# Optimization experiments

Measured on AMD Instinct MI355X. Metric: run time of the kernel, lower is better.

Reference implementation:

```python
import jax, jax.numpy as jnp
import numpy as np

N = 8192
IN_F = 512
OUT_F = 128
NUM_CLASSES = 10
ALPHA = 0.2  # LeakyReLU negative slope
NEG_INF = -9e15


def setup_inputs() -> dict:
    key = jax.random.key(0)
    k_h, k_d, k_W, k_a, k_cw, k_cb = jax.random.split(key, 6)
    h = jax.random.normal(k_h, (N, IN_F), dtype=jnp.float32)
    dist = jax.random.randint(k_d, (N, N), 0, 2, dtype=jnp.int32)
    # xavier_uniform with gain=1.414
    gain = 1.414
    lim_W = gain * np.sqrt(6.0 / (IN_F + OUT_F))
    W = jax.random.uniform(k_W, (IN_F, OUT_F), minval=-lim_W, maxval=lim_W, dtype=jnp.float32)
    lim_a = gain * np.sqrt(6.0 / (2 * OUT_F + 1))
    a = jax.random.uniform(k_a, (2 * OUT_F, 1), minval=-lim_a, maxval=lim_a, dtype=jnp.float32)
    # nn.Linear(out_features, num_classes): weight [C, out], bias [C]
    lim_c = np.sqrt(1.0 / OUT_F)
    Wc = jax.random.uniform(k_cw, (NUM_CLASSES, OUT_F), minval=-lim_c, maxval=lim_c, dtype=jnp.float32)
    bc = jax.random.uniform(k_cb, (NUM_CLASSES,), minval=-lim_c, maxval=lim_c, dtype=jnp.float32)
    return {"h": h, "dist": dist, "W": W, "a": a, "Wc": Wc, "bc": bc}


def reference(h, dist, W, a, Wc, bc):
    Wh = h @ W                              # [N, out]
    Wh1 = Wh @ a[:OUT_F]                    # [N, 1]
    Wh2 = Wh @ a[OUT_F:]                    # [N, 1]
    e = jax.nn.leaky_relu(Wh1 + Wh2.T, negative_slope=ALPHA)  # [N, N]
    att = jnp.where(dist > 0, e, NEG_INF)
    att = jax.nn.softmax(att, axis=1)       # [N, N]
    h_update = jax.nn.elu(att @ Wh)         # [N, out] (dropout inactive at inference)
    y_pred = h_update @ Wc.T + bc           # [N, num_classes]
    return y_pred
```

## Files before the change

### kernel.cpp

```cpp
#include <hip/hip_runtime.h>
#include <stdint.h>

#define N 8192
#define IN_F 512
#define OUT_F 128
#define NCLS 10
#define ALPHA 0.2f

#define WCOLS 1024
#define NSP (N / WCOLS)
#define BK 128
#define NIT (WCOLS / BK)
#define MSTR 33

typedef float f32x4 __attribute__((ext_vector_type(4)));
typedef int   i32x4 __attribute__((ext_vector_type(4)));
typedef short s16x8 __attribute__((ext_vector_type(8)));

__device__ __forceinline__ short f2bf(float x) {
    unsigned u = __builtin_bit_cast(unsigned, x);
    u = (u + 0x7FFFu + ((u >> 16) & 1u)) >> 16;
    return (short)u;
}
__device__ __forceinline__ float bf2f(short s) {
    unsigned u = ((unsigned)(unsigned short)s) << 16;
    return __builtin_bit_cast(float, u);
}

__global__ void split_w_kernel(const float* __restrict__ W,
                               short* __restrict__ WThi, short* __restrict__ WTlo) {
    int idx = blockIdx.x * 256 + threadIdx.x;
    int k = idx >> 7, col = idx & 127;
    float x = W[idx];
    short hi = f2bf(x);
    short lo = f2bf(x - bf2f(hi));
    size_t a = (size_t)(k >> 5) * (128 * 32) + (size_t)col * 32 + (k & 31);
    WThi[a] = hi;
    WTlo[a] = lo;
}

#define WH_ROWS 16
#define WH_STR 520

__global__ __launch_bounds__(256, 2)
void wh_kernel(const float* __restrict__ h, const short* __restrict__ WThi,
               const short* __restrict__ WTlo, const float* __restrict__ a,
               short* __restrict__ WhT, float* __restrict__ Wh1,
               float* __restrict__ Wh2) {
    __shared__ __align__(16) short Ahi[WH_ROWS][WH_STR];
    __shared__ __align__(16) short Alo[WH_ROWS][WH_STR];
    __shared__ __align__(16) float whs[WH_ROWS][OUT_F + 4];

    const int t = threadIdx.x;
    const int r0 = blockIdx.x * WH_ROWS;

    {
        int row = t >> 4, c4 = t & 15;
        const float* hrow = h + (size_t)(r0 + row) * IN_F;
        #pragma unroll
        for (int jj = 0; jj < 4; ++jj) {
            int k0 = c4 * 8 + jj * 128;
            f32x4 x0 = *(const f32x4*)(hrow + k0);
            f32x4 x1 = *(const f32x4*)(hrow + k0 + 4);
            s16x8 hi, lo;
            #pragma unroll
            for (int e = 0; e < 4; ++e) {
                short h0 = f2bf(x0[e]); hi[e] = h0; lo[e] = f2bf(x0[e] - bf2f(h0));
                short h1 = f2bf(x1[e]); hi[4 + e] = h1; lo[4 + e] = f2bf(x1[e] - bf2f(h1));
            }
            *(s16x8*)&Ahi[row][k0] = hi;
            *(s16x8*)&Alo[row][k0] = lo;
        }
    }
    __syncthreads();

    const int lane = t & 63, w = t >> 6;
    const int q = lane >> 4, ln16 = lane & 15;
    f32x4 acc[2] = {};
    #pragma unroll
    for (int kc = 0; kc < IN_F / 32; ++kc) {
        s16x8 ahi = *(const s16x8*)&Ahi[ln16][kc * 32 + q * 8];
        s16x8 alo = *(const s16x8*)&Alo[ln16][kc * 32 + q * 8];
        #pragma unroll
        for (int nt = 0; nt < 2; ++nt) {
            int col = w * 32 + nt * 16 + ln16;
            size_t boff = (size_t)kc * 4096 + (size_t)col * 32 + q * 8;
            s16x8 bhi = *(const s16x8*)(WThi + boff);
            s16x8 blo = *(const s16x8*)(WTlo + boff);
            acc[nt] = __builtin_amdgcn_mfma_f32_16x16x32_bf16(ahi, bhi, acc[nt], 0, 0, 0);
            acc[nt] = __builtin_amdgcn_mfma_f32_16x16x32_bf16(ahi, blo, acc[nt], 0, 0, 0);
            acc[nt] = __builtin_amdgcn_mfma_f32_16x16x32_bf16(alo, bhi, acc[nt], 0, 0, 0);
        }
    }
    #pragma unroll
    for (int nt = 0; nt < 2; ++nt)
        #pragma unroll
        for (int reg = 0; reg < 4; ++reg)
            whs[q * 4 + reg][w * 32 + nt * 16 + ln16] = acc[nt][reg];
    __syncthreads();

    if (t < 128) {
        int r = t >> 3, s = t & 7;
        float s1 = 0.f, s2 = 0.f;
        #pragma unroll
        for (int cc = 0; cc < 16; ++cc) {
            int c = s * 16 + cc;
            float v = whs[r][c];
            s1 = fmaf(v, a[c], s1);
            s2 = fmaf(v, a[OUT_F + c], s2);
        }
        s1 += __shfl_xor(s1, 1); s1 += __shfl_xor(s1, 2); s1 += __shfl_xor(s1, 4);
        s2 += __shfl_xor(s2, 1); s2 += __shfl_xor(s2, 2); s2 += __shfl_xor(s2, 4);
        if (s == 0) { Wh1[r0 + r] = s1; Wh2[r0 + r] = s2; }
    }

    {
        int c = t >> 1, h8 = t & 1;
        s16x8 pack;
        #pragma unroll
        for (int rr = 0; rr < 8; ++rr) pack[rr] = f2bf(whs[h8 * 8 + rr][c]);
        size_t addr = (size_t)(r0 >> 5) * 4096 + (size_t)c * 32 + (r0 & 16) + h8 * 8;
        *(s16x8*)(WhT + addr) = pack;
    }
}

__global__ __launch_bounds__(256, 4)
void attn_kernel(const int* __restrict__ dist, const short* __restrict__ WhT,
                 const float* __restrict__ Wh1v, const float* __restrict__ Wh2v,
                 float* __restrict__ acc_part, float* __restrict__ l_part) {
    __shared__ unsigned maskL[64 * MSTR];
    __shared__ __align__(16) float wh2L[WCOLS];

    const int t = threadIdx.x;
    const int it = blockIdx.x & 127;
    const int sp = blockIdx.x >> 7;
    const int i0 = it * 64;
    const int j0 = sp * WCOLS;
    const int lane = t & 63, w = t >> 6;
    const int q = lane >> 4, m = lane & 15;

    {
        const int l = lane;
        #pragma unroll 4
        for (int rr = 0; rr < 16; ++rr) {
            const int r = w * 16 + rr;
            const int* rp = dist + (size_t)(i0 + r) * N + j0 + l * 4;
            #pragma unroll
            for (int p = 0; p < 4; ++p) {
                i32x4 v = *(const i32x4*)(rp + p * 256);
                unsigned nib = (unsigned)(v[0] > 0) | ((unsigned)(v[1] > 0) << 1)
                             | ((unsigned)(v[2] > 0) << 2) | ((unsigned)(v[3] > 0) << 3);
                unsigned b = nib | (__shfl_xor(nib, 1) << 4);
                b = b | (__shfl_xor(b, 2) << 8);
                b = b | (__shfl_xor(b, 4) << 16);
                if ((l & 7) == 0) maskL[r * MSTR + p * 8 + (l >> 3)] = b;
            }
        }
        if (t < WCOLS / 4)
            *(f32x4*)&wh2L[t * 4] = *(const f32x4*)(Wh2v + j0 + t * 4);
    }
    __syncthreads();

    const int row = i0 + w * 16 + m;
    const float wh1 = Wh1v[row];
    float l_acc = 0.f;
    f32x4 acc[8] = {};
    const unsigned* mrow = &maskL[(w * 16 + m) * MSTR];

    for (int kt = 0; kt < NIT; ++kt) {
        const int jb = kt * BK;
        s16x8 afr[4];
        #pragma unroll
        for (int kc = 0; kc < 4; ++kc) {
            unsigned mw = mrow[(jb >> 5) + kc];
            unsigned byq = (mw >> (q * 8)) & 255u;
            f32x4 w20 = *(const f32x4*)&wh2L[jb + kc * 32 + q * 8];
            f32x4 w21 = *(const f32x4*)&wh2L[jb + kc * 32 + q * 8 + 4];
            #pragma unroll
            for (int e = 0; e < 4; ++e) {
                float sv = wh1 + w20[e];
                float lr = fmaxf(sv, ALPHA * sv);
                float pv = ((byq >> e) & 1u) ? __expf(lr) : 0.f;
                l_acc += pv;
                afr[kc][e] = (short)((__builtin_bit_cast(unsigned, pv) + 0x8000u) >> 16);
                float sv1 = wh1 + w21[e];
                float lr1 = fmaxf(sv1, ALPHA * sv1);
                float pv1 = ((byq >> (4 + e)) & 1u) ? __expf(lr1) : 0.f;
                l_acc += pv1;
                afr[kc][4 + e] = (short)((__builtin_bit_cast(unsigned, pv1) + 0x8000u) >> 16);
            }
        }
        const short* bb = WhT + (size_t)((j0 + jb) >> 5) * 4096 + q * 8;
        #pragma unroll
        for (int kc = 0; kc < 4; ++kc) {
            const short* bkc = bb + (size_t)kc * 4096;
            #pragma unroll
            for (int nt = 0; nt < 8; ++nt) {
                s16x8 bfr = *(const s16x8*)(bkc + (nt * 16 + m) * 32);
                acc[nt] = __builtin_amdgcn_mfma_f32_16x16x32_bf16(afr[kc], bfr, acc[nt], 0, 0, 0);
            }
        }
    }

    l_acc += __shfl_xor(l_acc, 16);
    l_acc += __shfl_xor(l_acc, 32);
    if (q == 0) l_part[(size_t)sp * N + row] = l_acc;

    float* ap = acc_part + (size_t)sp * N * OUT_F
              + ((size_t)i0 + w * 16 + q * 4) * OUT_F + m;
    #pragma unroll
    for (int reg = 0; reg < 4; ++reg)
        #pragma unroll
        for (int nt = 0; nt < 8; ++nt)
            ap[(size_t)reg * OUT_F + nt * 16] = acc[nt][reg];
}

__global__ __launch_bounds__(256, 4)
void reduce_kernel(const float* __restrict__ acc_part, const float* __restrict__ l_part,
                   const float* __restrict__ Wc, const float* __restrict__ bcv,
                   float* __restrict__ out) {
    __shared__ __align__(16) float hu[16][OUT_F + 4];
    const int t = threadIdx.x;
    const int i0 = blockIdx.x * 16;
    const int row = t >> 4, cg = t & 15;

    f32x4 v0 = {0.f, 0.f, 0.f, 0.f}, v1 = {0.f, 0.f, 0.f, 0.f};
    float l = 0.f;
    for (int s = 0; s < NSP; ++s) {
        const float* ap = acc_part + (size_t)s * N * OUT_F + (size_t)(i0 + row) * OUT_F + cg * 8;
        v0 += *(const f32x4*)ap;
        v1 += *(const f32x4*)(ap + 4);
        l += l_part[(size_t)s * N + i0 + row];
    }
    float inv = 1.f / l;
    #pragma unroll
    for (int e = 0; e < 4; ++e) {
        float x0 = v0[e] * inv; x0 = x0 > 0.f ? x0 : (__expf(x0) - 1.f);
        float x1 = v1[e] * inv; x1 = x1 > 0.f ? x1 : (__expf(x1) - 1.f);
        hu[row][cg * 8 + e] = x0;
        hu[row][cg * 8 + 4 + e] = x1;
    }
    __syncthreads();

    if (t < 16 * NCLS) {
        int rr = t / NCLS, cls = t - rr * NCLS;
        const f32x4* hurow = (const f32x4*)&hu[rr][0];
        const f32x4* wcrow = (const f32x4*)(Wc + cls * OUT_F);
        float sum = bcv[cls];
        #pragma unroll 8
        for (int c4 = 0; c4 < OUT_F / 4; ++c4) {
            f32x4 hv = hurow[c4];
            f32x4 wv = wcrow[c4];
            sum += hv[0] * wv[0] + hv[1] * wv[1] + hv[2] * wv[2] + hv[3] * wv[3];
        }
        out[(size_t)(i0 + rr) * NCLS + cls] = sum;
    }
}

extern "C" void kernel_launch(void* const* d_in, const int* in_sizes, int n_in,
                              void* d_out, int out_size, void* d_ws, size_t ws_size,
                              hipStream_t stream) {
    const float* h    = (const float*)d_in[0];
    const int*   dist = (const int*)d_in[1];
    const float* W    = (const float*)d_in[2];
    const float* a    = (const float*)d_in[3];
    const float* Wc   = (const float*)d_in[4];
    const float* bc   = (const float*)d_in[5];
    float* out = (float*)d_out;

    char* ws = (char*)d_ws;
    size_t off = 0;
    short* WhT  = (short*)(ws + off); off += (size_t)OUT_F * N * 2;
    short* WThi = (short*)(ws + off); off += (size_t)IN_F * OUT_F * 2;
    short* WTlo = (short*)(ws + off); off += (size_t)IN_F * OUT_F * 2;
    float* Wh1  = (float*)(ws + off); off += (size_t)N * 4;
    float* Wh2  = (float*)(ws + off); off += (size_t)N * 4;
    float* acc_part = (float*)(ws + off); off += (size_t)NSP * N * OUT_F * 4;
    float* l_part   = (float*)(ws + off);

    hipLaunchKernelGGL(split_w_kernel, dim3(256), dim3(256), 0, stream, W, WThi, WTlo);
    hipLaunchKernelGGL(wh_kernel, dim3(N / WH_ROWS), dim3(256), 0, stream,
                       h, WThi, WTlo, a, WhT, Wh1, Wh2);
    hipLaunchKernelGGL(attn_kernel, dim3(128 * NSP), dim3(256), 0, stream,
                       dist, WhT, Wh1, Wh2, acc_part, l_part);
    hipLaunchKernelGGL(reduce_kernel, dim3(N / 16), dim3(256), 0, stream,
                       acc_part, l_part, Wc, bc, out);
}
```

Baseline: 465.2 us.

## Pre-pack dist mask in separate kernel and split attention tile over output columns

Adds a dedicated pack kernel that streams the int32 adjacency matrix once and writes a bit-packed mask. The attention kernel then loads compact 32-bit mask words instead of reading and shuffling int32 data in its prologue. The attention tile shrinks to 32 rows, with waves split across two halves of the output columns, doubling the grid and raising occupancy to 6. The trade-offs are an extra launch, duplicated exp/softmax work across the column-split waves, and lower B-fragment reuse per block.

```diff
diff --git a/kernel.cpp b/kernel.cpp
--- a/kernel.cpp
+++ b/kernel.cpp
@@ -11,10 +11,10 @@
 #define NSP (N / WCOLS)
 #define BK 128
 #define NIT (WCOLS / BK)
-#define MSTR 33
 
 typedef float f32x4 __attribute__((ext_vector_type(4)));
 typedef int   i32x4 __attribute__((ext_vector_type(4)));
+typedef unsigned u32x4 __attribute__((ext_vector_type(4)));
 typedef short s16x8 __attribute__((ext_vector_type(8)));
 
 __device__ __forceinline__ short f2bf(float x) {
@@ -25,6 +25,27 @@
 __device__ __forceinline__ float bf2f(short s) {
     unsigned u = ((unsigned)(unsigned short)s) << 16;
     return __builtin_bit_cast(float, u);
+}
+
+__global__ __launch_bounds__(256)
+void pack_kernel(const int* __restrict__ dist, unsigned char* __restrict__ mask8) {
+    const int t = threadIdx.x;
+    const int row = blockIdx.x * 4 + (t >> 6);
+    const int l = t & 63;
+    const int* __restrict__ rp = dist + (size_t)row * N;
+    unsigned char* __restrict__ mp = mask8 + (size_t)row * (N / 8);
+
+    #pragma unroll 4
+    for (int c = 0; c < 16; ++c) {
+        const int jb = c * 512 + l * 8;
+        i32x4 v0 = *(const i32x4*)(rp + jb);
+        i32x4 v1 = *(const i32x4*)(rp + jb + 4);
+        unsigned b = (unsigned)(v0[0] > 0)       | ((unsigned)(v0[1] > 0) << 1)
+                   | ((unsigned)(v0[2] > 0) << 2) | ((unsigned)(v0[3] > 0) << 3)
+                   | ((unsigned)(v1[0] > 0) << 4) | ((unsigned)(v1[1] > 0) << 5)
+                   | ((unsigned)(v1[2] > 0) << 6) | ((unsigned)(v1[3] > 0) << 7);
+        mp[c * 64 + l] = (unsigned char)b;
+    }
 }
 
 __global__ void split_w_kernel(const float* __restrict__ W,
@@ -124,55 +145,42 @@
     }
 }
 
-__global__ __launch_bounds__(256, 4)
-void attn_kernel(const int* __restrict__ dist, const short* __restrict__ WhT,
+__global__ __launch_bounds__(256, 6)
+void attn_kernel(const unsigned* __restrict__ mask32, const short* __restrict__ WhT,
                  const float* __restrict__ Wh1v, const float* __restrict__ Wh2v,
                  float* __restrict__ acc_part, float* __restrict__ l_part) {
-    __shared__ unsigned maskL[64 * MSTR];
+    __shared__ unsigned maskW[32][33];
     __shared__ __align__(16) float wh2L[WCOLS];
 
     const int t = threadIdx.x;
-    const int it = blockIdx.x & 127;
-    const int sp = blockIdx.x >> 7;
-    const int i0 = it * 64;
+    const int it = blockIdx.x & 255;
+    const int sp = blockIdx.x >> 8;
+    const int i0 = it * 32;
     const int j0 = sp * WCOLS;
     const int lane = t & 63, w = t >> 6;
     const int q = lane >> 4, m = lane & 15;
-
-    {
-        const int l = lane;
-        #pragma unroll 4
-        for (int rr = 0; rr < 16; ++rr) {
-            const int r = w * 16 + rr;
-            const int* rp = dist + (size_t)(i0 + r) * N + j0 + l * 4;
-            #pragma unroll
-            for (int p = 0; p < 4; ++p) {
-                i32x4 v = *(const i32x4*)(rp + p * 256);
-                unsigned nib = (unsigned)(v[0] > 0) | ((unsigned)(v[1] > 0) << 1)
-                             | ((unsigned)(v[2] > 0) << 2) | ((unsigned)(v[3] > 0) << 3);
-                unsigned b = nib | (__shfl_xor(nib, 1) << 4);
-                b = b | (__shfl_xor(b, 2) << 8);
-                b = b | (__shfl_xor(b, 4) << 16);
-                if ((l & 7) == 0) maskL[r * MSTR + p * 8 + (l >> 3)] = b;
-            }
-        }
-        if (t < WCOLS / 4)
-            *(f32x4*)&wh2L[t * 4] = *(const f32x4*)(Wh2v + j0 + t * 4);
-    }
-    __syncthreads();
-
-    const int row = i0 + w * 16 + m;
-    const float wh1 = Wh1v[row];
+    const int rh = w >> 1, nh = w & 1;
+
+    #pragma unroll
+    for (int ii = 0; ii < 4; ++ii) {
+        int idx = t + ii * 256;
+        int r = idx >> 5, wq = idx & 31;
+        maskW[r][wq] = mask32[(size_t)(i0 + r) * (N / 32) + (j0 >> 5) + wq];
+    }
+    *(f32x4*)&wh2L[t * 4] = *(const f32x4*)(Wh2v + j0 + t * 4);
+    __syncthreads();
+
+    const int rowm = rh * 16 + m;
+    const float wh1 = Wh1v[i0 + rowm];
     float l_acc = 0.f;
-    f32x4 acc[8] = {};
-    const unsigned* mrow = &maskL[(w * 16 + m) * MSTR];
+    f32x4 acc[4] = {};
 
     for (int kt = 0; kt < NIT; ++kt) {
         const int jb = kt * BK;
         s16x8 afr[4];
         #pragma unroll
         for (int kc = 0; kc < 4; ++kc) {
-            unsigned mw = mrow[(jb >> 5) + kc];
+            unsigned mw = maskW[rowm][(jb >> 5) + kc];
             unsigned byq = (mw >> (q * 8)) & 255u;
             f32x4 w20 = *(const f32x4*)&wh2L[jb + kc * 32 + q * 8];
             f32x4 w21 = *(const f32x4*)&wh2L[jb + kc * 32 + q * 8 + 4];
@@ -195,8 +203,8 @@
         for (int kc = 0; kc < 4; ++kc) {
             const short* bkc = bb + (size_t)kc * 4096;
             #pragma unroll
-            for (int nt = 0; nt < 8; ++nt) {
-                s16x8 bfr = *(const s16x8*)(bkc + (nt * 16 + m) * 32);
+            for (int nt = 0; nt < 4; ++nt) {
+                s16x8 bfr = *(const s16x8*)(bkc + (nh * 64 + nt * 16 + m) * 32);
                 acc[nt] = __builtin_amdgcn_mfma_f32_16x16x32_bf16(afr[kc], bfr, acc[nt], 0, 0, 0);
             }
         }
@@ -204,14 +212,14 @@
 
     l_acc += __shfl_xor(l_acc, 16);
     l_acc += __shfl_xor(l_acc, 32);
-    if (q == 0) l_part[(size_t)sp * N + row] = l_acc;
+    if (q == 0 && nh == 0) l_part[(size_t)sp * N + i0 + rowm] = l_acc;
 
     float* ap = acc_part + (size_t)sp * N * OUT_F
-              + ((size_t)i0 + w * 16 + q * 4) * OUT_F + m;
+              + ((size_t)i0 + rh * 16 + q * 4) * OUT_F + nh * 64 + m;
     #pragma unroll
     for (int reg = 0; reg < 4; ++reg)
         #pragma unroll
-        for (int nt = 0; nt < 8; ++nt)
+        for (int nt = 0; nt < 4; ++nt)
             ap[(size_t)reg * OUT_F + nt * 16] = acc[nt][reg];
 }
 
@@ -275,14 +283,16 @@
     short* WTlo = (short*)(ws + off); off += (size_t)IN_F * OUT_F * 2;
     float* Wh1  = (float*)(ws + off); off += (size_t)N * 4;
     float* Wh2  = (float*)(ws + off); off += (size_t)N * 4;
+    unsigned char* mask8 = (unsigned char*)(ws + off); off += (size_t)N * (N / 8);
     float* acc_part = (float*)(ws + off); off += (size_t)NSP * N * OUT_F * 4;
     float* l_part   = (float*)(ws + off);
 
+    hipLaunchKernelGGL(pack_kernel, dim3(N / 4), dim3(256), 0, stream, dist, mask8);
     hipLaunchKernelGGL(split_w_kernel, dim3(256), dim3(256), 0, stream, W, WThi, WTlo);
     hipLaunchKernelGGL(wh_kernel, dim3(N / WH_ROWS), dim3(256), 0, stream,
                        h, WThi, WTlo, a, WhT, Wh1, Wh2);
-    hipLaunchKernelGGL(attn_kernel, dim3(128 * NSP), dim3(256), 0, stream,
-                       dist, WhT, Wh1, Wh2, acc_part, l_part);
+    hipLaunchKernelGGL(attn_kernel, dim3(256 * NSP), dim3(256), 0, stream,
+                       (const unsigned*)mask8, WhT, Wh1, Wh2, acc_part, l_part);
     hipLaunchKernelGGL(reduce_kernel, dim3(N / 16), dim3(256), 0, stream,
                        acc_part, l_part, Wc, bc, out);
 }
```

After: 487.2 us. 1.05x slower.
